# Optimization experiments

Measured on AMD Instinct MI355X. Metric: run time of the kernel, lower is better.

Reference implementation:

```python
import jax, jax.numpy as jnp
import numpy as np
from jax import lax

N = 4096
T = 8192
DT = 0.1
C_M = 1.0
E_REST = 0.0
G_M_LEAK = 5.0
I_BIAS = 0.0


def setup_inputs() -> dict:
    key = jax.random.key(0)
    i_ext_vector = jax.random.normal(key, (N, T), dtype=jnp.float32)
    return {"i_ext_vector": i_ext_vector}


def reference(i_ext_vector) -> jnp.ndarray:
    # RK2 (modified Euler) integration of leaky non-spiking neuron dynamics.
    # dv/dt = (i_bias + i_ext - (v - e_rest) * g_m_leak) / c_m
    def dvdt(v, i_ext):
        return (I_BIAS + i_ext - (v - E_REST) * G_M_LEAK) / C_M

    def step(v, i_t):
        k1 = dvdt(v, i_t)
        k2 = dvdt(v + 0.5 * DT * k1, i_t)
        v_new = v + DT * k2
        return v_new, v_new

    v0 = jnp.full((N,), E_REST, dtype=i_ext_vector.dtype)
    # scan over time: i_ext_vector is (N, T) -> scan over leading axis of (T, N)
    _, v_hist = lax.scan(step, v0, i_ext_vector.T)  # v_hist: (T, N)
    return v_hist.T  # (N, T), matches v_m_Post
```

## Files before the change

### kernel.cpp

```cpp
#include <hip/hip_runtime.h>


typedef float fx4 __attribute__((ext_vector_type(4)));

constexpr int TT  = 8192;
constexpr int BLK = 256;
constexpr int SEG = 512;
constexpr int WPB = BLK / 64;

__global__ __launch_bounds__(BLK, 8)
void neuron_scan(const float* __restrict__ in, float* __restrict__ out,
                 int nseg) {
    const float A   = 0.625f;
    const float Bc  = 0.075f;
    const float A4  = 0.152587890625f;
    const float A8  = 2.32830643653869629e-2f;
    const float A16 = 5.42101086242752217e-4f;
    const float A32 = 2.93873587705571877e-7f;
    const float A64 = 8.63616855509444e-14f;

    const int lane = threadIdx.x & 63;
    const int wid  = blockIdx.x * WPB + (threadIdx.x >> 6);
    const int nw   = gridDim.x * WPB;

    for (int s = wid; s < nseg; s += nw) {
        const int row = s >> 4;
        const int col = s & 15;
        const size_t base = (size_t)row * TT + (size_t)col * SEG;
        const fx4* src = (const fx4*)(in + base);

        fx4 x0 = src[2 * lane];
        fx4 x1 = src[2 * lane + 1];

        float vwarm = 0.0f;
        if (col > 0) {
            fx4 wx = {0.0f, 0.0f, 0.0f, 0.0f};
            if (lane < 16) wx = src[lane - 16];
            float cw;
            cw = Bc * wx.x;
            cw = fmaf(A, cw, Bc * wx.y);
            cw = fmaf(A, cw, Bc * wx.z);
            cw = fmaf(A, cw, Bc * wx.w);
            float u;
            u = __shfl_up(cw, 1); if (lane >= 1) cw = fmaf(A4,  u, cw);
            u = __shfl_up(cw, 2); if (lane >= 2) cw = fmaf(A8,  u, cw);
            u = __shfl_up(cw, 4); if (lane >= 4) cw = fmaf(A16, u, cw);
            u = __shfl_up(cw, 8); if (lane >= 8) cw = fmaf(A32, u, cw);
            vwarm = __shfl(cw, 15);
        }

        float c;
        c = Bc * x0.x;
        c = fmaf(A, c, Bc * x0.y);
        c = fmaf(A, c, Bc * x0.z);
        c = fmaf(A, c, Bc * x0.w);
        c = fmaf(A, c, Bc * x1.x);
        c = fmaf(A, c, Bc * x1.y);
        c = fmaf(A, c, Bc * x1.z);
        c = fmaf(A, c, Bc * x1.w);
        if (lane == 0) c = fmaf(A8, vwarm, c);

        float u;
        u = __shfl_up(c, 1); if (lane >= 1) c = fmaf(A8,  u, c);
        u = __shfl_up(c, 2); if (lane >= 2) c = fmaf(A16, u, c);
        u = __shfl_up(c, 4); if (lane >= 4) c = fmaf(A32, u, c);
        u = __shfl_up(c, 8); if (lane >= 8) c = fmaf(A64, u, c);

        float venter = __shfl_up(c, 1);
        if (lane == 0) venter = vwarm;

        float v = venter;
        fx4 o0, o1;
        v = fmaf(A, v, Bc * x0.x); o0.x = v;
        v = fmaf(A, v, Bc * x0.y); o0.y = v;
        v = fmaf(A, v, Bc * x0.z); o0.z = v;
        v = fmaf(A, v, Bc * x0.w); o0.w = v;
        v = fmaf(A, v, Bc * x1.x); o1.x = v;
        v = fmaf(A, v, Bc * x1.y); o1.y = v;
        v = fmaf(A, v, Bc * x1.z); o1.z = v;
        v = fmaf(A, v, Bc * x1.w); o1.w = v;

        fx4* dst = (fx4*)(out + base);
        __builtin_nontemporal_store(o0, dst + 2 * lane);
        __builtin_nontemporal_store(o1, dst + 2 * lane + 1);
    }
}

extern "C" void kernel_launch(void* const* d_in, const int* in_sizes, int n_in,
                              void* d_out, int out_size, void* d_ws, size_t ws_size,
                              hipStream_t stream) {
    const float* in = (const float*)d_in[0];
    float* out = (float*)d_out;
    const int n_rows = in_sizes[0] / TT;
    const int nseg = n_rows * (TT / SEG);
    int blocks = 2048;
    if (blocks * WPB > nseg) blocks = (nseg + WPB - 1) / WPB;
    neuron_scan<<<dim3(blocks), dim3(BLK), 0, stream>>>(in, out, nseg);
}
```

Measured before the change: 236.3 us.

## Double scan segment length to 1024 and use regular stores

Each wavefront now handles a 1024-element segment, with 16 elements per lane instead of 8. This halves the number of segments and the per-segment warmup loads and shuffle scans, and the decay constants shift accordingly (A16..A128). The nontemporal output stores are replaced with plain stores. Each lane's 64-byte stride is less coalesced per instruction and register use rises, which may lower occupancy.

```diff
diff --git a/kernel.cpp b/kernel.cpp
--- a/kernel.cpp
+++ b/kernel.cpp
@@ -5,32 +5,35 @@
 
 constexpr int TT  = 8192;
 constexpr int BLK = 256;
-constexpr int SEG = 512;
+constexpr int SEG = 1024;
 constexpr int WPB = BLK / 64;
 
 __global__ __launch_bounds__(BLK, 8)
 void neuron_scan(const float* __restrict__ in, float* __restrict__ out,
                  int nseg) {
-    const float A   = 0.625f;
-    const float Bc  = 0.075f;
-    const float A4  = 0.152587890625f;
-    const float A8  = 2.32830643653869629e-2f;
-    const float A16 = 5.42101086242752217e-4f;
-    const float A32 = 2.93873587705571877e-7f;
-    const float A64 = 8.63616855509444e-14f;
+    const float A    = 0.625f;
+    const float Bc   = 0.075f;
+    const float A4   = 0.152587890625f;
+    const float A8   = 2.32830643653869629e-2f;
+    const float A16  = 5.42101086242752217e-4f;
+    const float A32  = 2.93873587705571877e-7f;
+    const float A64  = 8.63616855509444463e-14f;
+    const float A128 = 7.45834073120020674e-27f;
 
     const int lane = threadIdx.x & 63;
     const int wid  = blockIdx.x * WPB + (threadIdx.x >> 6);
     const int nw   = gridDim.x * WPB;
 
     for (int s = wid; s < nseg; s += nw) {
-        const int row = s >> 4;
-        const int col = s & 15;
+        const int row = s >> 3;
+        const int col = s & 7;
         const size_t base = (size_t)row * TT + (size_t)col * SEG;
         const fx4* src = (const fx4*)(in + base);
 
-        fx4 x0 = src[2 * lane];
-        fx4 x1 = src[2 * lane + 1];
+        fx4 x0 = src[4 * lane];
+        fx4 x1 = src[4 * lane + 1];
+        fx4 x2 = src[4 * lane + 2];
+        fx4 x3 = src[4 * lane + 3];
 
         float vwarm = 0.0f;
         if (col > 0) {
@@ -58,31 +61,48 @@
         c = fmaf(A, c, Bc * x1.y);
         c = fmaf(A, c, Bc * x1.z);
         c = fmaf(A, c, Bc * x1.w);
-        if (lane == 0) c = fmaf(A8, vwarm, c);
+        c = fmaf(A, c, Bc * x2.x);
+        c = fmaf(A, c, Bc * x2.y);
+        c = fmaf(A, c, Bc * x2.z);
+        c = fmaf(A, c, Bc * x2.w);
+        c = fmaf(A, c, Bc * x3.x);
+        c = fmaf(A, c, Bc * x3.y);
+        c = fmaf(A, c, Bc * x3.z);
+        c = fmaf(A, c, Bc * x3.w);
+        if (lane == 0) c = fmaf(A16, vwarm, c);
 
         float u;
-        u = __shfl_up(c, 1); if (lane >= 1) c = fmaf(A8,  u, c);
-        u = __shfl_up(c, 2); if (lane >= 2) c = fmaf(A16, u, c);
-        u = __shfl_up(c, 4); if (lane >= 4) c = fmaf(A32, u, c);
-        u = __shfl_up(c, 8); if (lane >= 8) c = fmaf(A64, u, c);
+        u = __shfl_up(c, 1); if (lane >= 1) c = fmaf(A16,  u, c);
+        u = __shfl_up(c, 2); if (lane >= 2) c = fmaf(A32,  u, c);
+        u = __shfl_up(c, 4); if (lane >= 4) c = fmaf(A64,  u, c);
+        u = __shfl_up(c, 8); if (lane >= 8) c = fmaf(A128, u, c);
 
         float venter = __shfl_up(c, 1);
         if (lane == 0) venter = vwarm;
 
         float v = venter;
-        fx4 o0, o1;
-        v = fmaf(A, v, Bc * x0.x); o0.x = v;
-        v = fmaf(A, v, Bc * x0.y); o0.y = v;
-        v = fmaf(A, v, Bc * x0.z); o0.z = v;
-        v = fmaf(A, v, Bc * x0.w); o0.w = v;
-        v = fmaf(A, v, Bc * x1.x); o1.x = v;
-        v = fmaf(A, v, Bc * x1.y); o1.y = v;
-        v = fmaf(A, v, Bc * x1.z); o1.z = v;
-        v = fmaf(A, v, Bc * x1.w); o1.w = v;
+        v = fmaf(A, v, Bc * x0.x); x0.x = v;
+        v = fmaf(A, v, Bc * x0.y); x0.y = v;
+        v = fmaf(A, v, Bc * x0.z); x0.z = v;
+        v = fmaf(A, v, Bc * x0.w); x0.w = v;
+        v = fmaf(A, v, Bc * x1.x); x1.x = v;
+        v = fmaf(A, v, Bc * x1.y); x1.y = v;
+        v = fmaf(A, v, Bc * x1.z); x1.z = v;
+        v = fmaf(A, v, Bc * x1.w); x1.w = v;
+        v = fmaf(A, v, Bc * x2.x); x2.x = v;
+        v = fmaf(A, v, Bc * x2.y); x2.y = v;
+        v = fmaf(A, v, Bc * x2.z); x2.z = v;
+        v = fmaf(A, v, Bc * x2.w); x2.w = v;
+        v = fmaf(A, v, Bc * x3.x); x3.x = v;
+        v = fmaf(A, v, Bc * x3.y); x3.y = v;
+        v = fmaf(A, v, Bc * x3.z); x3.z = v;
+        v = fmaf(A, v, Bc * x3.w); x3.w = v;
 
         fx4* dst = (fx4*)(out + base);
-        __builtin_nontemporal_store(o0, dst + 2 * lane);
-        __builtin_nontemporal_store(o1, dst + 2 * lane + 1);
+        dst[4 * lane]     = x0;
+        dst[4 * lane + 1] = x1;
+        dst[4 * lane + 2] = x2;
+        dst[4 * lane + 3] = x3;
     }
 }
 
```

Measured after the change: 237.3 us. No clear change (+0.4%).

## Widen per-wave segment to 2048 elements with 32 values per lane

Applied to the files above, without the earlier changes.

Each wave now processes a 2048-element segment, with 8 float4 vectors per lane instead of 2, so the cross-lane shuffle scan needs only 3 steps and the 16-element warm-up overhead is paid four times less often per row. The warm-up load is issued early, alongside the main loads. Output stores switch from nontemporal to regular stores, and the launch uses fewer blocks with lower occupancy bounds. The cost is more registers per thread and fewer waves in flight to hide memory latency in a bandwidth-bound kernel.

```diff
diff --git a/kernel.cpp b/kernel.cpp
--- a/kernel.cpp
+++ b/kernel.cpp
@@ -5,37 +5,51 @@
 
 constexpr int TT  = 8192;
 constexpr int BLK = 256;
-constexpr int SEG = 512;
+constexpr int SEG = 2048;
+constexpr int NV  = 8;
 constexpr int WPB = BLK / 64;
 
-__global__ __launch_bounds__(BLK, 8)
+__global__ __launch_bounds__(BLK, 4)
 void neuron_scan(const float* __restrict__ in, float* __restrict__ out,
                  int nseg) {
-    const float A   = 0.625f;
-    const float Bc  = 0.075f;
-    const float A4  = 0.152587890625f;
-    const float A8  = 2.32830643653869629e-2f;
-    const float A16 = 5.42101086242752217e-4f;
-    const float A32 = 2.93873587705571877e-7f;
-    const float A64 = 8.63616855509444e-14f;
+    const float A    = 0.625f;
+    const float Bc   = 0.075f;
+    const float A4   = 0.152587890625f;
+    const float A8   = 2.32830643653869629e-2f;
+    const float A16  = 5.42101086242752217e-4f;
+    const float A32  = 2.93873587705571877e-7f;
+    const float A64  = 8.63616855509444463e-14f;
+    const float A128 = 7.45834073120020674e-27f;
 
     const int lane = threadIdx.x & 63;
     const int wid  = blockIdx.x * WPB + (threadIdx.x >> 6);
     const int nw   = gridDim.x * WPB;
 
     for (int s = wid; s < nseg; s += nw) {
-        const int row = s >> 4;
-        const int col = s & 15;
+        const int row = s >> 2;
+        const int col = s & 3;
         const size_t base = (size_t)row * TT + (size_t)col * SEG;
         const fx4* src = (const fx4*)(in + base);
 
-        fx4 x0 = src[2 * lane];
-        fx4 x1 = src[2 * lane + 1];
+        fx4 x[NV];
+        #pragma unroll
+        for (int k = 0; k < NV; ++k) x[k] = src[NV * lane + k];
+
+        const bool wu = (col > 0);
+        fx4 wx = {0.0f, 0.0f, 0.0f, 0.0f};
+        if (wu && lane < 16) wx = src[lane - 16];
+
+        float c = 0.0f;
+        #pragma unroll
+        for (int k = 0; k < NV; ++k) {
+            c = fmaf(A, c, Bc * x[k].x);
+            c = fmaf(A, c, Bc * x[k].y);
+            c = fmaf(A, c, Bc * x[k].z);
+            c = fmaf(A, c, Bc * x[k].w);
+        }
 
         float vwarm = 0.0f;
-        if (col > 0) {
-            fx4 wx = {0.0f, 0.0f, 0.0f, 0.0f};
-            if (lane < 16) wx = src[lane - 16];
+        if (wu) {
             float cw;
             cw = Bc * wx.x;
             cw = fmaf(A, cw, Bc * wx.y);
@@ -48,41 +62,28 @@
             u = __shfl_up(cw, 8); if (lane >= 8) cw = fmaf(A32, u, cw);
             vwarm = __shfl(cw, 15);
         }
-
-        float c;
-        c = Bc * x0.x;
-        c = fmaf(A, c, Bc * x0.y);
-        c = fmaf(A, c, Bc * x0.z);
-        c = fmaf(A, c, Bc * x0.w);
-        c = fmaf(A, c, Bc * x1.x);
-        c = fmaf(A, c, Bc * x1.y);
-        c = fmaf(A, c, Bc * x1.z);
-        c = fmaf(A, c, Bc * x1.w);
-        if (lane == 0) c = fmaf(A8, vwarm, c);
+        if (lane == 0) c = fmaf(A32, vwarm, c);
 
         float u;
-        u = __shfl_up(c, 1); if (lane >= 1) c = fmaf(A8,  u, c);
-        u = __shfl_up(c, 2); if (lane >= 2) c = fmaf(A16, u, c);
-        u = __shfl_up(c, 4); if (lane >= 4) c = fmaf(A32, u, c);
-        u = __shfl_up(c, 8); if (lane >= 8) c = fmaf(A64, u, c);
+        u = __shfl_up(c, 1); if (lane >= 1) c = fmaf(A32,  u, c);
+        u = __shfl_up(c, 2); if (lane >= 2) c = fmaf(A64,  u, c);
+        u = __shfl_up(c, 4); if (lane >= 4) c = fmaf(A128, u, c);
 
         float venter = __shfl_up(c, 1);
         if (lane == 0) venter = vwarm;
 
         float v = venter;
-        fx4 o0, o1;
-        v = fmaf(A, v, Bc * x0.x); o0.x = v;
-        v = fmaf(A, v, Bc * x0.y); o0.y = v;
-        v = fmaf(A, v, Bc * x0.z); o0.z = v;
-        v = fmaf(A, v, Bc * x0.w); o0.w = v;
-        v = fmaf(A, v, Bc * x1.x); o1.x = v;
-        v = fmaf(A, v, Bc * x1.y); o1.y = v;
-        v = fmaf(A, v, Bc * x1.z); o1.z = v;
-        v = fmaf(A, v, Bc * x1.w); o1.w = v;
+        #pragma unroll
+        for (int k = 0; k < NV; ++k) {
+            v = fmaf(A, v, Bc * x[k].x); x[k].x = v;
+            v = fmaf(A, v, Bc * x[k].y); x[k].y = v;
+            v = fmaf(A, v, Bc * x[k].z); x[k].z = v;
+            v = fmaf(A, v, Bc * x[k].w); x[k].w = v;
+        }
 
         fx4* dst = (fx4*)(out + base);
-        __builtin_nontemporal_store(o0, dst + 2 * lane);
-        __builtin_nontemporal_store(o1, dst + 2 * lane + 1);
+        #pragma unroll
+        for (int k = 0; k < NV; ++k) dst[NV * lane + k] = x[k];
     }
 }
 
@@ -93,7 +94,7 @@
     float* out = (float*)d_out;
     const int n_rows = in_sizes[0] / TT;
     const int nseg = n_rows * (TT / SEG);
-    int blocks = 2048;
+    int blocks = 1024;
     if (blocks * WPB > nseg) blocks = (nseg + WPB - 1) / WPB;
     neuron_scan<<<dim3(blocks), dim3(BLK), 0, stream>>>(in, out, nseg);
 }
```

Result: no change. 240.3 us (+1.7%).
